# Performance work log

Measured on AMD Instinct MI355X. Metric: run time of the kernel, lower is better.

The kernel has to match this reference:

```python
import jax, jax.numpy as jnp
import numpy as np

ATT_RAW = 312
HID = 900
ATT_DIM = 4096


def setup_inputs() -> dict:
    key = jax.random.key(0)
    ks = jax.random.split(key, 12)
    B, S, N, C = 4, 128, 50, ATT_DIM
    x = jax.random.normal(ks[0], (B, S, C), dtype=jnp.float32)
    x_label = jax.random.randint(ks[1], (B, S), 0, N, dtype=jnp.int64)
    att = jax.random.normal(ks[2], (B, N, ATT_RAW), dtype=jnp.float32)
    att_label = jax.random.randint(ks[3], (B, N), 0, N, dtype=jnp.int64)
    def lin(k, out_f, in_f):
        bound = 1.0 / np.sqrt(in_f)
        kw, kb = jax.random.split(k)
        W = jax.random.uniform(kw, (out_f, in_f), jnp.float32, -bound, bound)
        b = jax.random.uniform(kb, (out_f,), jnp.float32, -bound, bound)
        return W, b
    W1, b1 = lin(ks[4], HID, ATT_RAW)       # attnet layer 1
    W2, b2 = lin(ks[5], ATT_DIM, HID)       # attnet layer 2
    W3, b3 = lin(ks[6], HID, 2 * ATT_DIM)   # o layer 1
    W4, b4 = lin(ks[7], 1, HID)             # o layer 2
    return {"x": x, "x_label": x_label, "att": att, "att_label": att_label,
            "W1": W1, "b1": b1, "W2": W2, "b2": b2,
            "W3": W3, "b3": b3, "W4": W4, "b4": b4}


def reference(x, x_label, att, att_label, W1, b1, W2, b2, W3, b3, W4, b4):
    # x: [B,S,C], att: [B,N,312]; train=True branch -> scalar MSE loss
    B, S, C = x.shape
    N = att.shape[1]
    # attnet: 312 -> 900 -> 4096 with ReLU
    att_f = jax.nn.relu(jax.nn.relu(att @ W1.T + b1) @ W2.T + b2)  # [B,N,4096]
    # o layer 1 on concat([x_f, att_f]) == split matmul + broadcast add
    W3x, W3a = W3[:, :C], W3[:, C:]
    hx = jnp.einsum('bsc,hc->bsh', x, W3x)        # [B,S,900]
    ha = jnp.einsum('bnc,hc->bnh', att_f, W3a)    # [B,N,900]
    pre = jax.nn.relu(hx[:, :, None, :] + ha[:, None, :, :] + b3)  # [B,S,N,900]
    score = jax.nn.sigmoid(jnp.einsum('bsnh,h->bsn', pre, W4[0]) + b4[0])  # [B,S,N]
    label = (x_label[:, :, None] == att_label[:, None, :]).astype(score.dtype)
    loss = jnp.sum((label - score) ** 2) / B / S
    return loss
```

## Files before the change

### kernel.cpp

```cpp
#include <hip/hip_runtime.h>
#include <hip/hip_bf16.h>

typedef __attribute__((ext_vector_type(8))) short bf16x8;
typedef __attribute__((ext_vector_type(4))) float f32x4;
typedef __attribute__((ext_vector_type(8))) unsigned short u16x8;

__device__ __forceinline__ void gload16(const void* g, void* l) {
    __builtin_amdgcn_global_load_lds((const __attribute__((address_space(1))) void*)g,
                                     (__attribute__((address_space(3))) void*)l, 16, 0, 0);
}

__device__ __forceinline__ float bf2f(unsigned short u) {
    union { unsigned i; float f; } v; v.i = ((unsigned)u) << 16; return v.f;
}

struct PadJob {
    const float* src; unsigned short* dst;
    int src_ld, col0, M, K, Kp;
    int chunk_begin;
};
struct PadJobs { PadJob j[6]; int total; };

__global__ __launch_bounds__(256)
void padconv6(PadJobs P)
{
    const int idx = blockIdx.x * 256 + threadIdx.x;
    if (idx >= P.total) return;
    int ji = 0;
    #pragma unroll
    for (int k = 1; k < 6; ++k) if (idx >= P.j[k].chunk_begin) ji = k;
    const PadJob J = P.j[ji];
    const int cid = idx - J.chunk_begin;
    const int kp8 = J.Kp >> 3;
    const int m = cid / kp8;
    const int kc = (cid - m * kp8) << 3;
    u16x8 v;
    if (m < J.M && kc + 8 <= J.K) {
        const float* s = J.src + (size_t)m * J.src_ld + J.col0 + kc;
        const float4 f0 = *(const float4*)s;
        const float4 f1 = *(const float4*)(s + 4);
        const float ff[8] = {f0.x, f0.y, f0.z, f0.w, f1.x, f1.y, f1.z, f1.w};
        #pragma unroll
        for (int j = 0; j < 8; ++j) {
            __hip_bfloat16 h = __float2bfloat16(ff[j]);
            v[j] = *(unsigned short*)&h;
        }
    } else {
        #pragma unroll
        for (int j = 0; j < 8; ++j) {
            float f = 0.f;
            const int k = kc + j;
            if (m < J.M && k < J.K) f = J.src[(size_t)m * J.src_ld + J.col0 + k];
            __hip_bfloat16 h = __float2bfloat16(f);
            v[j] = *(unsigned short*)&h;
        }
    }
    *(u16x8*)(J.dst + (size_t)m * J.Kp + kc) = v;
}

template<bool RELU, bool BIAS>
__global__ __launch_bounds__(256)
void gemm_mfma64(const unsigned short* __restrict__ A,
                 const unsigned short* __restrict__ B,
                 const float* __restrict__ bias,
                 unsigned short* __restrict__ Cout, int ldc,
                 int Mtrue, int Ntrue, int Kp)
{
    __shared__ short As[64 * 64];
    __shared__ short Bs[64 * 64];
    const int bm = blockIdx.y * 64, bn = blockIdx.x * 64;
    const int tid = threadIdx.x;
    const int w = tid >> 6, l = tid & 63;
    const int wm = w >> 1, wn = w & 1;

    const int sr0 = w * 8 + (l >> 3);
    const int scb = (l & 7) * 16;

    f32x4 acc[2][2];
    #pragma unroll
    for (int i = 0; i < 2; ++i)
        #pragma unroll
        for (int j = 0; j < 2; ++j)
            acc[i][j] = (f32x4){0.f, 0.f, 0.f, 0.f};

    for (int k0 = 0; k0 < Kp; k0 += 64) {
        #pragma unroll
        for (int c = 0; c < 2; ++c) {
            const int r = c * 32 + sr0;
            const int cbs = scb ^ ((r & 7) << 4);
            const char* ga = (const char*)(A + (size_t)(bm + r) * Kp + k0) + cbs;
            const char* gb = (const char*)(B + (size_t)(bn + r) * Kp + k0) + cbs;
            char* la = (char*)As + (size_t)(c * 32 + w * 8) * 128;
            char* lb = (char*)Bs + (size_t)(c * 32 + w * 8) * 128;
            gload16(ga, la);
            gload16(gb, lb);
        }
        asm volatile("s_waitcnt vmcnt(0)");
        __syncthreads();

        #pragma unroll
        for (int ks = 0; ks < 64; ks += 32) {
            bf16x8 a[2], b[2];
            const int kb = ks * 2 + (l >> 4) * 16;
            #pragma unroll
            for (int i = 0; i < 2; ++i) {
                const int ra = wm * 32 + i * 16 + (l & 15);
                a[i] = *(const bf16x8*)((const char*)As + ra * 128 + (kb ^ ((ra & 7) << 4)));
                const int rb = wn * 32 + i * 16 + (l & 15);
                b[i] = *(const bf16x8*)((const char*)Bs + rb * 128 + (kb ^ ((rb & 7) << 4)));
            }
            #pragma unroll
            for (int i = 0; i < 2; ++i)
                #pragma unroll
                for (int j = 0; j < 2; ++j)
                    acc[i][j] = __builtin_amdgcn_mfma_f32_16x16x32_bf16(a[i], b[j], acc[i][j], 0, 0, 0);
        }
        __syncthreads();
    }

    #pragma unroll
    for (int i = 0; i < 2; ++i) {
        #pragma unroll
        for (int j = 0; j < 2; ++j) {
            const int col = bn + wn * 32 + j * 16 + (l & 15);
            float bv = 0.f;
            if (BIAS && col < Ntrue) bv = bias[col];
            #pragma unroll
            for (int q = 0; q < 4; ++q) {
                const int row = bm + wm * 32 + i * 16 + (l >> 4) * 4 + q;
                float v = acc[i][j][q] + bv;
                if (RELU) v = fmaxf(v, 0.f);
                if (row >= Mtrue) v = 0.f;
                __hip_bfloat16 h = __float2bfloat16(v);
                Cout[(size_t)row * ldc + col] = *(unsigned short*)&h;
            }
        }
    }
}

struct G34Args {
    const unsigned short *A3, *B3; float* P3;
    const unsigned short *A4, *B4; float* P4;
};

__global__ __launch_bounds__(256)
void gemm128_split(G34Args ga)
{
    __shared__ short As[128 * 64];
    __shared__ short Bs[128 * 64];
    const int tid = threadIdx.x;
    const int w = tid >> 6, l = tid & 63;
    const int wm = w >> 1, wn = w & 1;

    const unsigned short *A, *Bm;
    float* P;
    int by, bx, z, Mtrue;
    const int gid = blockIdx.x;
    if (gid < 256) {
        z = gid >> 5; const int rem = gid & 31; by = rem >> 3; bx = rem & 7;
        A = ga.A3; Bm = ga.B3; P = ga.P3; Mtrue = 512;
    } else {
        const int g2 = gid - 256;
        z = g2 >> 4; const int rem = g2 & 15; by = rem >> 3; bx = rem & 7;
        A = ga.A4; Bm = ga.B4; P = ga.P4; Mtrue = 200;
    }
    const int Kp = 4096;
    const int k_begin = z * 512;

    const int sr0 = w * 8 + (l >> 3);
    const int scb = (l & 7) * 16;
    const int swa = scb ^ ((sr0 & 7) << 4);

    f32x4 acc[4][4];
    #pragma unroll
    for (int i = 0; i < 4; ++i)
        #pragma unroll
        for (int j = 0; j < 4; ++j)
            acc[i][j] = (f32x4){0.f, 0.f, 0.f, 0.f};

    for (int k0 = k_begin; k0 < k_begin + 512; k0 += 64) {
        #pragma unroll
        for (int c = 0; c < 4; ++c) {
            const int r = c * 32 + sr0;
            const char* gA = (const char*)(A  + (size_t)(by * 128 + r) * Kp + k0) + swa;
            const char* gB = (const char*)(Bm + (size_t)(bx * 128 + r) * Kp + k0) + swa;
            char* la = (char*)As + (size_t)(c * 32 + w * 8) * 128;
            char* lb = (char*)Bs + (size_t)(c * 32 + w * 8) * 128;
            gload16(gA, la);
            gload16(gB, lb);
        }
        asm volatile("s_waitcnt vmcnt(0)");
        __syncthreads();

        #pragma unroll
        for (int ks = 0; ks < 64; ks += 32) {
            bf16x8 a[4], b[4];
            const int kb = ks * 2 + (l >> 4) * 16;
            #pragma unroll
            for (int i = 0; i < 4; ++i) {
                const int ra = wm * 64 + i * 16 + (l & 15);
                a[i] = *(const bf16x8*)((const char*)As + ra * 128 + (kb ^ ((ra & 7) << 4)));
                const int rb = wn * 64 + i * 16 + (l & 15);
                b[i] = *(const bf16x8*)((const char*)Bs + rb * 128 + (kb ^ ((rb & 7) << 4)));
            }
            #pragma unroll
            for (int i = 0; i < 4; ++i)
                #pragma unroll
                for (int j = 0; j < 4; ++j)
                    acc[i][j] = __builtin_amdgcn_mfma_f32_16x16x32_bf16(a[i], b[j], acc[i][j], 0, 0, 0);
        }
        __syncthreads();
    }

    float* slab = P + (size_t)z * Mtrue * 900;
    #pragma unroll
    for (int i = 0; i < 4; ++i) {
        #pragma unroll
        for (int j = 0; j < 4; ++j) {
            const int col = bx * 128 + wn * 64 + j * 16 + (l & 15);
            if (col >= 900) continue;
            #pragma unroll
            for (int q = 0; q < 4; ++q) {
                const int row = by * 128 + wm * 64 + i * 16 + (l >> 4) * 4 + q;
                if (row < Mtrue)
                    slab[(size_t)row * 900 + col] = acc[i][j][q];
            }
        }
    }
}

__global__ __launch_bounds__(256)
void reduce_both(const float* __restrict__ hxp, const float* __restrict__ hap,
                 const float* __restrict__ b3,
                 unsigned short* __restrict__ hx_bf, unsigned short* __restrict__ ha_bf)
{
    int idx = blockIdx.x * 256 + threadIdx.x;
    const int HX = 512 * 113;
    const float* p; unsigned short* o; const float* bias; int M, m;
    if (idx < HX) { p = hxp; o = hx_bf; bias = b3; M = 512; }
    else {
        idx -= HX;
        if (idx >= 200 * 113) return;
        p = hap; o = ha_bf; bias = nullptr; M = 200;
    }
    m = idx / 113;
    const int c = idx - m * 113;
    const int k = c * 8;
    u16x8 v;
    #pragma unroll
    for (int q = 0; q < 8; q += 4) {
        if (k + q < 900) {
            float4 a = *(const float4*)(p + (size_t)m * 900 + k + q);
            #pragma unroll 1
            for (int s = 1; s < 8; ++s) {
                const float4 t = *(const float4*)(p + ((size_t)s * M + m) * 900 + k + q);
                a.x += t.x; a.y += t.y; a.z += t.z; a.w += t.w;
            }
            if (bias) {
                const float4 bb = *(const float4*)(bias + k + q);
                a.x += bb.x; a.y += bb.y; a.z += bb.z; a.w += bb.w;
            }
            const float ff[4] = {a.x, a.y, a.z, a.w};
            #pragma unroll
            for (int j = 0; j < 4; ++j) {
                __hip_bfloat16 h = __float2bfloat16(ff[j]);
                v[q + j] = *(unsigned short*)&h;
            }
        } else {
            #pragma unroll
            for (int j = 0; j < 4; ++j) v[q + j] = 0;
        }
    }
    *(u16x8*)(o + (size_t)m * 904 + k) = v;
}

__global__ __launch_bounds__(512)
void score_loss(const unsigned short* __restrict__ hxb,
                const unsigned short* __restrict__ hab,
                const float* __restrict__ W4,
                const float* __restrict__ b4,
                const int* __restrict__ xl,
                const int* __restrict__ al,
                float* __restrict__ part)
{
    __shared__ __align__(16) unsigned short hxs[8 * 904];
    __shared__ __align__(16) unsigned short has[16 * 904];
    __shared__ __align__(16) float w4s[904];
    __shared__ float zpart[4][8][16];
    __shared__ float red[2];

    const int tid = threadIdx.x;
    const int nt = blockIdx.x, st = blockIdx.y, b = blockIdx.z;
    const int row0 = b * 128 + st * 8;

    for (int t = tid; t < 24 * 113; t += 512) {
        u16x8 v;
        unsigned short* dst;
        if (t < 8 * 113) {
            const int r = t / 113, c = t - r * 113;
            v = *(const u16x8*)(hxb + (size_t)(row0 + r) * 904 + c * 8);
            dst = hxs + r * 904 + c * 8;
        } else {
            const int t2 = t - 8 * 113;
            const int r = t2 / 113, c = t2 - r * 113;
            const int n = nt * 16 + r;
            if (n < 50) v = *(const u16x8*)(hab + (size_t)(b * 50 + n) * 904 + c * 8);
            else        v = (u16x8){0,0,0,0,0,0,0,0};
            dst = has + r * 904 + c * 8;
        }
        *(u16x8*)dst = v;
    }
    for (int t = tid; t < 226; t += 512) {
        float4 v = {0.f, 0.f, 0.f, 0.f};
        if (t < 225) v = *(const float4*)(W4 + t * 4);
        *(float4*)(w4s + t * 4) = v;
    }
    __syncthreads();

    const int hs = tid >> 7;
    const int si = (tid >> 4) & 7;
    const int ni = tid & 15;

    float acc = 0.f;
    const unsigned short* hrow = hxs + si * 904;
    const unsigned short* arow = has + ni * 904;
    for (int c = hs; c < 113; c += 4) {
        const u16x8 hv = *(const u16x8*)(hrow + c * 8);
        const u16x8 av = *(const u16x8*)(arow + c * 8);
        const float4 w0 = *(const float4*)(w4s + c * 8);
        const float4 w1 = *(const float4*)(w4s + c * 8 + 4);
        const float ww[8] = {w0.x, w0.y, w0.z, w0.w, w1.x, w1.y, w1.z, w1.w};
        #pragma unroll
        for (int j = 0; j < 8; ++j) {
            const float u = bf2f((unsigned short)hv[j]) + bf2f((unsigned short)av[j]);
            acc = fmaf(fmaxf(u, 0.f), ww[j], acc);
        }
    }
    zpart[hs][si][ni] = acc;
    __syncthreads();

    float dd = 0.f;
    if (tid < 128) {
        const int esi = tid >> 4, eni = tid & 15;
        const int n = nt * 16 + eni;
        const float z = zpart[0][esi][eni] + zpart[1][esi][eni]
                      + zpart[2][esi][eni] + zpart[3][esi][eni] + b4[0];
        const float sc = 1.f / (1.f + __expf(-z));
        if (n < 50) {
            const float lab = (xl[row0 + esi] == al[b * 50 + n]) ? 1.f : 0.f;
            const float d = lab - sc;
            dd = d * d;
        }
        #pragma unroll
        for (int off = 32; off > 0; off >>= 1)
            dd += __shfl_down(dd, off);
        if ((tid & 63) == 0) red[tid >> 6] = dd;
    }
    __syncthreads();
    if (tid == 0)
        part[nt + 4 * (st + 16 * b)] = red[0] + red[1];
}

__global__ __launch_bounds__(256)
void final_loss(const float* __restrict__ part, float* __restrict__ out)
{
    __shared__ float r[4];
    const int tid = threadIdx.x;
    float v = part[tid];
    #pragma unroll
    for (int off = 32; off > 0; off >>= 1)
        v += __shfl_down(v, off);
    if ((tid & 63) == 0) r[tid >> 6] = v;
    __syncthreads();
    if (tid == 0) out[0] = (r[0] + r[1] + r[2] + r[3]) * (1.f / 512.f);
}

extern "C" void kernel_launch(void* const* d_in, const int* in_sizes, int n_in,
                              void* d_out, int out_size, void* d_ws, size_t ws_size,
                              hipStream_t stream)
{
    const float* x   = (const float*)d_in[0];
    const int*   xl  = (const int*)  d_in[1];
    const float* att = (const float*)d_in[2];
    const int*   al  = (const int*)  d_in[3];
    const float* W1  = (const float*)d_in[4];
    const float* b1  = (const float*)d_in[5];
    const float* W2  = (const float*)d_in[6];
    const float* b2  = (const float*)d_in[7];
    const float* W3  = (const float*)d_in[8];
    const float* b3  = (const float*)d_in[9];
    const float* W4  = (const float*)d_in[10];
    const float* b4  = (const float*)d_in[11];
    float* out = (float*)d_out;

    const int B = 4, S = 128, N = 50, C = 4096, H = 900, AR = 312;
    const int MS = B * S;
    const int MN = B * N;
    const int MNp = 256;
    const int ARp = 320, Hp = 960;
    const int W3p = 1024;
    const int SPLITS = 8;

    char* base = (char*)d_ws;
    size_t off = 0;
    auto alloc = [&](size_t bytes) { void* r = base + off; off = (off + bytes + 255) & ~(size_t)255; return r; };
    unsigned short* x_bf   = (unsigned short*)alloc((size_t)MS * C * 2);
    unsigned short* att_bf = (unsigned short*)alloc((size_t)MNp * ARp * 2);
    unsigned short* W1_bf  = (unsigned short*)alloc((size_t)Hp * ARp * 2);
    unsigned short* W2_bf  = (unsigned short*)alloc((size_t)C * Hp * 2);
    unsigned short* W3x_bf = (unsigned short*)alloc((size_t)W3p * C * 2);
    unsigned short* W3a_bf = (unsigned short*)alloc((size_t)W3p * C * 2);
    unsigned short* h1_bf  = (unsigned short*)alloc((size_t)MNp * Hp * 2);
    unsigned short* attf_bf= (unsigned short*)alloc((size_t)MNp * C * 2);
    float* hxp = (float*)alloc((size_t)SPLITS * MS * H * 4);
    float* hap = (float*)alloc((size_t)SPLITS * MN * H * 4);
    unsigned short* hx_bf = (unsigned short*)alloc((size_t)MS * 904 * 2);
    unsigned short* ha_bf = (unsigned short*)alloc((size_t)MN * 904 * 2);
    float* part = (float*)alloc(256 * 4);

    const dim3 blk(256);
    auto cdiv = [](int a, int b) { return (a + b - 1) / b; };

    PadJobs P;
    int cb = 0;
    auto setjob = [&](int i, const float* src, unsigned short* dst, int ld, int col0,
                      int M, int K, int Kp, int Mp) {
        P.j[i] = PadJob{src, dst, ld, col0, M, K, Kp, cb};
        cb += Mp * (Kp >> 3);
    };
    setjob(0, x,   x_bf,   C,     0, MS, C,  C,   MS);
    setjob(1, att, att_bf, AR,    0, MN, AR, ARp, MNp);
    setjob(2, W1,  W1_bf,  AR,    0, H,  AR, ARp, Hp);
    setjob(3, W2,  W2_bf,  H,     0, C,  H,  Hp,  C);
    setjob(4, W3,  W3x_bf, 2 * C, 0, H,  C,  C,   W3p);
    setjob(5, W3,  W3a_bf, 2 * C, C, H,  C,  C,   W3p);
    P.total = cb;
    padconv6<<<cdiv(cb, 256), blk, 0, stream>>>(P);

    gemm_mfma64<true, true><<<dim3(Hp / 64, MNp / 64), blk, 0, stream>>>(
        att_bf, W1_bf, b1, h1_bf, Hp, MN, H, ARp);

    gemm_mfma64<true, true><<<dim3(C / 64, MNp / 64), blk, 0, stream>>>(
        h1_bf, W2_bf, b2, attf_bf, C, MN, C, Hp);

    G34Args ga{x_bf, W3x_bf, hxp, attf_bf, W3a_bf, hap};
    gemm128_split<<<dim3(384), blk, 0, stream>>>(ga);

    reduce_both<<<cdiv((MS + MN) * 113, 256), blk, 0, stream>>>(hxp, hap, b3, hx_bf, ha_bf);

    score_loss<<<dim3(4, 16, 4), dim3(512), 0, stream>>>(hx_bf, ha_bf, W4, b4, xl, al, part);
    final_loss<<<dim3(1), blk, 0, stream>>>(part, out);
}
```

Measured before the change: 71.24 us.

## Fuse fp32-to-bf16 conversion and padding into GEMM tile staging

Removes the separate padconv6 pre-pass that converted x, att, W1, W2 and W3 into padded bf16 workspace copies. Each GEMM now reads the fp32 (or bf16) source directly, converts and zero-pads in registers, and writes into swizzled LDS. This avoids a full extra write and read of about 30 MB of converted data and one kernel launch. In exchange it drops the asynchronous global_load_lds path for ordinary register-staged loads with bounds checks, and the fp32 sources double the bytes read per tile.

```diff
diff --git a/kernel.cpp b/kernel.cpp
--- a/kernel.cpp
+++ b/kernel.cpp
@@ -5,63 +5,58 @@
 typedef __attribute__((ext_vector_type(4))) float f32x4;
 typedef __attribute__((ext_vector_type(8))) unsigned short u16x8;
 
-__device__ __forceinline__ void gload16(const void* g, void* l) {
-    __builtin_amdgcn_global_load_lds((const __attribute__((address_space(1))) void*)g,
-                                     (__attribute__((address_space(3))) void*)l, 16, 0, 0);
-}
-
 __device__ __forceinline__ float bf2f(unsigned short u) {
     union { unsigned i; float f; } v; v.i = ((unsigned)u) << 16; return v.f;
 }
-
-struct PadJob {
-    const float* src; unsigned short* dst;
-    int src_ld, col0, M, K, Kp;
-    int chunk_begin;
-};
-struct PadJobs { PadJob j[6]; int total; };
-
-__global__ __launch_bounds__(256)
-void padconv6(PadJobs P)
-{
-    const int idx = blockIdx.x * 256 + threadIdx.x;
-    if (idx >= P.total) return;
-    int ji = 0;
-    #pragma unroll
-    for (int k = 1; k < 6; ++k) if (idx >= P.j[k].chunk_begin) ji = k;
-    const PadJob J = P.j[ji];
-    const int cid = idx - J.chunk_begin;
-    const int kp8 = J.Kp >> 3;
-    const int m = cid / kp8;
-    const int kc = (cid - m * kp8) << 3;
-    u16x8 v;
-    if (m < J.M && kc + 8 <= J.K) {
-        const float* s = J.src + (size_t)m * J.src_ld + J.col0 + kc;
-        const float4 f0 = *(const float4*)s;
-        const float4 f1 = *(const float4*)(s + 4);
-        const float ff[8] = {f0.x, f0.y, f0.z, f0.w, f1.x, f1.y, f1.z, f1.w};
-        #pragma unroll
-        for (int j = 0; j < 8; ++j) {
-            __hip_bfloat16 h = __float2bfloat16(ff[j]);
-            v[j] = *(unsigned short*)&h;
-        }
-    } else {
-        #pragma unroll
-        for (int j = 0; j < 8; ++j) {
-            float f = 0.f;
-            const int k = kc + j;
-            if (m < J.M && k < J.K) f = J.src[(size_t)m * J.src_ld + J.col0 + k];
-            __hip_bfloat16 h = __float2bfloat16(f);
-            v[j] = *(unsigned short*)&h;
-        }
-    }
-    *(u16x8*)(J.dst + (size_t)m * J.Kp + kc) = v;
+__device__ __forceinline__ unsigned short f2bf(float f) {
+    __hip_bfloat16 h = __float2bfloat16(f);
+    return *(unsigned short*)&h;
+}
+
+template<int ROWS>
+__device__ __forceinline__ void stage_tile(
+    const void* __restrict__ src, int ld, int isbf, int row0, int rmax,
+    int k0, int kmax, short* __restrict__ lds, int tid)
+{
+    #pragma unroll
+    for (int i = 0; i < ROWS / 32; ++i) {
+        const int ch = i * 256 + tid;
+        const int r = ch >> 3;
+        const int kc8 = (ch & 7) * 8;
+        const int gr = row0 + r;
+        const int gk = k0 + kc8;
+        u16x8 v;
+        if (gr < rmax && gk + 8 <= kmax) {
+            if (isbf) {
+                v = *(const u16x8*)((const unsigned short*)src + (size_t)gr * ld + gk);
+            } else {
+                const float* s = (const float*)src + (size_t)gr * ld + gk;
+                const float4 f0 = *(const float4*)s;
+                const float4 f1 = *(const float4*)(s + 4);
+                const float ff[8] = {f0.x, f0.y, f0.z, f0.w, f1.x, f1.y, f1.z, f1.w};
+                #pragma unroll
+                for (int j = 0; j < 8; ++j) v[j] = f2bf(ff[j]);
+            }
+        } else if (gr < rmax && gk < kmax) {
+            #pragma unroll
+            for (int j = 0; j < 8; ++j) {
+                float f = 0.f;
+                if (gk + j < kmax)
+                    f = isbf ? bf2f(((const unsigned short*)src)[(size_t)gr * ld + gk + j])
+                             : ((const float*)src)[(size_t)gr * ld + gk + j];
+                v[j] = f2bf(f);
+            }
+        } else {
+            v = (u16x8){0, 0, 0, 0, 0, 0, 0, 0};
+        }
+        *(u16x8*)((char*)lds + r * 128 + ((kc8 * 2) ^ ((r & 7) << 4))) = v;
+    }
 }
 
 template<bool RELU, bool BIAS>
 __global__ __launch_bounds__(256)
-void gemm_mfma64(const unsigned short* __restrict__ A,
-                 const unsigned short* __restrict__ B,
+void gemm_mfma64(const void* __restrict__ A, int lda, int a_bf, int a_rmax, int a_kmax,
+                 const void* __restrict__ B, int ldb, int b_bf, int b_rmax, int b_kmax,
                  const float* __restrict__ bias,
                  unsigned short* __restrict__ Cout, int ldc,
                  int Mtrue, int Ntrue, int Kp)
@@ -73,9 +68,6 @@
     const int w = tid >> 6, l = tid & 63;
     const int wm = w >> 1, wn = w & 1;
 
-    const int sr0 = w * 8 + (l >> 3);
-    const int scb = (l & 7) * 16;
-
     f32x4 acc[2][2];
     #pragma unroll
     for (int i = 0; i < 2; ++i)
@@ -84,18 +76,8 @@
             acc[i][j] = (f32x4){0.f, 0.f, 0.f, 0.f};
 
     for (int k0 = 0; k0 < Kp; k0 += 64) {
-        #pragma unroll
-        for (int c = 0; c < 2; ++c) {
-            const int r = c * 32 + sr0;
-            const int cbs = scb ^ ((r & 7) << 4);
-            const char* ga = (const char*)(A + (size_t)(bm + r) * Kp + k0) + cbs;
-            const char* gb = (const char*)(B + (size_t)(bn + r) * Kp + k0) + cbs;
-            char* la = (char*)As + (size_t)(c * 32 + w * 8) * 128;
-            char* lb = (char*)Bs + (size_t)(c * 32 + w * 8) * 128;
-            gload16(ga, la);
-            gload16(gb, lb);
-        }
-        asm volatile("s_waitcnt vmcnt(0)");
+        stage_tile<64>(A, lda, a_bf, bm, a_rmax, k0, a_kmax, As, tid);
+        stage_tile<64>(B, ldb, b_bf, bn, b_rmax, k0, b_kmax, Bs, tid);
         __syncthreads();
 
         #pragma unroll
@@ -131,16 +113,15 @@
                 float v = acc[i][j][q] + bv;
                 if (RELU) v = fmaxf(v, 0.f);
                 if (row >= Mtrue) v = 0.f;
-                __hip_bfloat16 h = __float2bfloat16(v);
-                Cout[(size_t)row * ldc + col] = *(unsigned short*)&h;
+                Cout[(size_t)row * ldc + col] = f2bf(v);
             }
         }
     }
 }
 
 struct G34Args {
-    const unsigned short *A3, *B3; float* P3;
-    const unsigned short *A4, *B4; float* P4;
+    const void *A3; const float *B3; float* P3;
+    const void *A4; const float *B4; float* P4;
 };
 
 __global__ __launch_bounds__(256)
@@ -152,24 +133,19 @@
     const int w = tid >> 6, l = tid & 63;
     const int wm = w >> 1, wn = w & 1;
 
-    const unsigned short *A, *Bm;
+    const void *A; const float *Bm;
     float* P;
-    int by, bx, z, Mtrue;
+    int by, bx, z, Mtrue, a_bf, a_rmax, lda;
     const int gid = blockIdx.x;
     if (gid < 256) {
         z = gid >> 5; const int rem = gid & 31; by = rem >> 3; bx = rem & 7;
-        A = ga.A3; Bm = ga.B3; P = ga.P3; Mtrue = 512;
+        A = ga.A3; Bm = ga.B3; P = ga.P3; Mtrue = 512; a_bf = 0; a_rmax = 512; lda = 4096;
     } else {
         const int g2 = gid - 256;
         z = g2 >> 4; const int rem = g2 & 15; by = rem >> 3; bx = rem & 7;
-        A = ga.A4; Bm = ga.B4; P = ga.P4; Mtrue = 200;
-    }
-    const int Kp = 4096;
+        A = ga.A4; Bm = ga.B4; P = ga.P4; Mtrue = 200; a_bf = 1; a_rmax = 256; lda = 4096;
+    }
     const int k_begin = z * 512;
-
-    const int sr0 = w * 8 + (l >> 3);
-    const int scb = (l & 7) * 16;
-    const int swa = scb ^ ((sr0 & 7) << 4);
 
     f32x4 acc[4][4];
     #pragma unroll
@@ -179,17 +155,8 @@
             acc[i][j] = (f32x4){0.f, 0.f, 0.f, 0.f};
 
     for (int k0 = k_begin; k0 < k_begin + 512; k0 += 64) {
-        #pragma unroll
-        for (int c = 0; c < 4; ++c) {
-            const int r = c * 32 + sr0;
-            const char* gA = (const char*)(A  + (size_t)(by * 128 + r) * Kp + k0) + swa;
-            const char* gB = (const char*)(Bm + (size_t)(bx * 128 + r) * Kp + k0) + swa;
-            char* la = (char*)As + (size_t)(c * 32 + w * 8) * 128;
-            char* lb = (char*)Bs + (size_t)(c * 32 + w * 8) * 128;
-            gload16(gA, la);
-            gload16(gB, lb);
-        }
-        asm volatile("s_waitcnt vmcnt(0)");
+        stage_tile<128>(A, lda, a_bf, by * 128, a_rmax, k0, 4096, As, tid);
+        stage_tile<128>(Bm, 8192, 0, bx * 128, 900, k0, 1 << 30, Bs, tid);
         __syncthreads();
 
         #pragma unroll
@@ -260,12 +227,8 @@
                 const float4 bb = *(const float4*)(bias + k + q);
                 a.x += bb.x; a.y += bb.y; a.z += bb.z; a.w += bb.w;
             }
-            const float ff[4] = {a.x, a.y, a.z, a.w};
-            #pragma unroll
-            for (int j = 0; j < 4; ++j) {
-                __hip_bfloat16 h = __float2bfloat16(ff[j]);
-                v[q + j] = *(unsigned short*)&h;
-            }
+            v[q + 0] = f2bf(a.x); v[q + 1] = f2bf(a.y);
+            v[q + 2] = f2bf(a.z); v[q + 3] = f2bf(a.w);
         } else {
             #pragma unroll
             for (int j = 0; j < 4; ++j) v[q + j] = 0;
@@ -398,18 +361,11 @@
     const int MN = B * N;
     const int MNp = 256;
     const int ARp = 320, Hp = 960;
-    const int W3p = 1024;
     const int SPLITS = 8;
 
     char* base = (char*)d_ws;
     size_t off = 0;
     auto alloc = [&](size_t bytes) { void* r = base + off; off = (off + bytes + 255) & ~(size_t)255; return r; };
-    unsigned short* x_bf   = (unsigned short*)alloc((size_t)MS * C * 2);
-    unsigned short* att_bf = (unsigned short*)alloc((size_t)MNp * ARp * 2);
-    unsigned short* W1_bf  = (unsigned short*)alloc((size_t)Hp * ARp * 2);
-    unsigned short* W2_bf  = (unsigned short*)alloc((size_t)C * Hp * 2);
-    unsigned short* W3x_bf = (unsigned short*)alloc((size_t)W3p * C * 2);
-    unsigned short* W3a_bf = (unsigned short*)alloc((size_t)W3p * C * 2);
     unsigned short* h1_bf  = (unsigned short*)alloc((size_t)MNp * Hp * 2);
     unsigned short* attf_bf= (unsigned short*)alloc((size_t)MNp * C * 2);
     float* hxp = (float*)alloc((size_t)SPLITS * MS * H * 4);
@@ -421,29 +377,17 @@
     const dim3 blk(256);
     auto cdiv = [](int a, int b) { return (a + b - 1) / b; };
 
-    PadJobs P;
-    int cb = 0;
-    auto setjob = [&](int i, const float* src, unsigned short* dst, int ld, int col0,
-                      int M, int K, int Kp, int Mp) {
-        P.j[i] = PadJob{src, dst, ld, col0, M, K, Kp, cb};
-        cb += Mp * (Kp >> 3);
-    };
-    setjob(0, x,   x_bf,   C,     0, MS, C,  C,   MS);
-    setjob(1, att, att_bf, AR,    0, MN, AR, ARp, MNp);
-    setjob(2, W1,  W1_bf,  AR,    0, H,  AR, ARp, Hp);
-    setjob(3, W2,  W2_bf,  H,     0, C,  H,  Hp,  C);
-    setjob(4, W3,  W3x_bf, 2 * C, 0, H,  C,  C,   W3p);
-    setjob(5, W3,  W3a_bf, 2 * C, C, H,  C,  C,   W3p);
-    P.total = cb;
-    padconv6<<<cdiv(cb, 256), blk, 0, stream>>>(P);
-
     gemm_mfma64<true, true><<<dim3(Hp / 64, MNp / 64), blk, 0, stream>>>(
-        att_bf, W1_bf, b1, h1_bf, Hp, MN, H, ARp);
+        att, AR, 0, MN, AR,
+        W1,  AR, 0, H,  AR,
+        b1, h1_bf, Hp, MN, H, ARp);
 
     gemm_mfma64<true, true><<<dim3(C / 64, MNp / 64), blk, 0, stream>>>(
-        h1_bf, W2_bf, b2, attf_bf, C, MN, C, Hp);
-
-    G34Args ga{x_bf, W3x_bf, hxp, attf_bf, W3a_bf, hap};
+        h1_bf, Hp, 1, MNp, Hp,
+        W2,    H,  0, C,   H,
+        b2, attf_bf, C, MN, C, Hp);
+
+    G34Args ga{x, W3, hxp, attf_bf, W3 + C, hap};
     gemm128_split<<<dim3(384), blk, 0, stream>>>(ga);
 
     reduce_both<<<cdiv((MS + MN) * 113, 256), blk, 0, stream>>>(hxp, hap, b3, hx_bf, ha_bf);
```

Measured after the change: 94.22 us. 32.2% more time.

## Double-buffer LDS in GEMM kernels and raise split-K for the x-side GEMM

Applied to the files above, without the earlier changes.

Both MFMA GEMM kernels now use two LDS buffers and issue the global-to-LDS loads for the next K tile before computing the current one, so memory latency overlaps with MFMA work. The x-side GEMM in the split kernel goes from 8 to 16 K-splits (640 blocks instead of 384), which adds parallelism across CUs. The cost is twice the fp32 partial-sum traffic and reduction work for hx, plus higher LDS use per block (64KB in the split kernel), which may lower occupancy.

```diff
diff --git a/kernel.cpp b/kernel.cpp
--- a/kernel.cpp
+++ b/kernel.cpp
@@ -9,9 +9,12 @@
     __builtin_amdgcn_global_load_lds((const __attribute__((address_space(1))) void*)g,
                                      (__attribute__((address_space(3))) void*)l, 16, 0, 0);
 }
-
 __device__ __forceinline__ float bf2f(unsigned short u) {
     union { unsigned i; float f; } v; v.i = ((unsigned)u) << 16; return v.f;
+}
+__device__ __forceinline__ unsigned short f2bf(float f) {
+    __hip_bfloat16 h = __float2bfloat16(f);
+    return *(unsigned short*)&h;
 }
 
 struct PadJob {
@@ -41,21 +44,34 @@
         const float4 f1 = *(const float4*)(s + 4);
         const float ff[8] = {f0.x, f0.y, f0.z, f0.w, f1.x, f1.y, f1.z, f1.w};
         #pragma unroll
-        for (int j = 0; j < 8; ++j) {
-            __hip_bfloat16 h = __float2bfloat16(ff[j]);
-            v[j] = *(unsigned short*)&h;
-        }
+        for (int j = 0; j < 8; ++j) v[j] = f2bf(ff[j]);
     } else {
         #pragma unroll
         for (int j = 0; j < 8; ++j) {
             float f = 0.f;
             const int k = kc + j;
             if (m < J.M && k < J.K) f = J.src[(size_t)m * J.src_ld + J.col0 + k];
-            __hip_bfloat16 h = __float2bfloat16(f);
-            v[j] = *(unsigned short*)&h;
+            v[j] = f2bf(f);
         }
     }
     *(u16x8*)(J.dst + (size_t)m * J.Kp + kc) = v;
+}
+
+template<int ROWS>
+__device__ __forceinline__ void stage_gl(const unsigned short* __restrict__ src,
+                                         int ld, int row0, int k0,
+                                         short* __restrict__ lds, int w, int l)
+{
+    const int sr0 = w * 8 + (l >> 3);
+    const int scb = (l & 7) * 16;
+    #pragma unroll
+    for (int c = 0; c < ROWS / 32; ++c) {
+        const int r = c * 32 + sr0;
+        const int cbs = scb ^ ((r & 7) << 4);
+        const char* g = (const char*)(src + (size_t)(row0 + r) * ld + k0) + cbs;
+        char* dst = (char*)lds + (size_t)(c * 32 + w * 8) * 128;
+        gload16(g, dst);
+    }
 }
 
 template<bool RELU, bool BIAS>
@@ -66,15 +82,13 @@
                  unsigned short* __restrict__ Cout, int ldc,
                  int Mtrue, int Ntrue, int Kp)
 {
-    __shared__ short As[64 * 64];
-    __shared__ short Bs[64 * 64];
+    __shared__ short As[2][64 * 64];
+    __shared__ short Bs[2][64 * 64];
     const int bm = blockIdx.y * 64, bn = blockIdx.x * 64;
     const int tid = threadIdx.x;
     const int w = tid >> 6, l = tid & 63;
     const int wm = w >> 1, wn = w & 1;
-
-    const int sr0 = w * 8 + (l >> 3);
-    const int scb = (l & 7) * 16;
+    const int nk = Kp >> 6;
 
     f32x4 acc[2][2];
     #pragma unroll
@@ -83,21 +97,17 @@
         for (int j = 0; j < 2; ++j)
             acc[i][j] = (f32x4){0.f, 0.f, 0.f, 0.f};
 
-    for (int k0 = 0; k0 < Kp; k0 += 64) {
-        #pragma unroll
-        for (int c = 0; c < 2; ++c) {
-            const int r = c * 32 + sr0;
-            const int cbs = scb ^ ((r & 7) << 4);
-            const char* ga = (const char*)(A + (size_t)(bm + r) * Kp + k0) + cbs;
-            const char* gb = (const char*)(B + (size_t)(bn + r) * Kp + k0) + cbs;
-            char* la = (char*)As + (size_t)(c * 32 + w * 8) * 128;
-            char* lb = (char*)Bs + (size_t)(c * 32 + w * 8) * 128;
-            gload16(ga, la);
-            gload16(gb, lb);
-        }
-        asm volatile("s_waitcnt vmcnt(0)");
-        __syncthreads();
-
+    stage_gl<64>(A, Kp, bm, 0, As[0], w, l);
+    stage_gl<64>(B, Kp, bn, 0, Bs[0], w, l);
+    asm volatile("s_waitcnt vmcnt(0)");
+    __syncthreads();
+
+    int cur = 0;
+    for (int t = 0; t < nk; ++t) {
+        if (t + 1 < nk) {
+            stage_gl<64>(A, Kp, bm, (t + 1) * 64, As[cur ^ 1], w, l);
+            stage_gl<64>(B, Kp, bn, (t + 1) * 64, Bs[cur ^ 1], w, l);
+        }
         #pragma unroll
         for (int ks = 0; ks < 64; ks += 32) {
             bf16x8 a[2], b[2];
@@ -105,9 +115,9 @@
             #pragma unroll
             for (int i = 0; i < 2; ++i) {
                 const int ra = wm * 32 + i * 16 + (l & 15);
-                a[i] = *(const bf16x8*)((const char*)As + ra * 128 + (kb ^ ((ra & 7) << 4)));
+                a[i] = *(const bf16x8*)((const char*)As[cur] + ra * 128 + (kb ^ ((ra & 7) << 4)));
                 const int rb = wn * 32 + i * 16 + (l & 15);
-                b[i] = *(const bf16x8*)((const char*)Bs + rb * 128 + (kb ^ ((rb & 7) << 4)));
+                b[i] = *(const bf16x8*)((const char*)Bs[cur] + rb * 128 + (kb ^ ((rb & 7) << 4)));
             }
             #pragma unroll
             for (int i = 0; i < 2; ++i)
@@ -115,7 +125,9 @@
                 for (int j = 0; j < 2; ++j)
                     acc[i][j] = __builtin_amdgcn_mfma_f32_16x16x32_bf16(a[i], b[j], acc[i][j], 0, 0, 0);
         }
+        asm volatile("s_waitcnt vmcnt(0)");
         __syncthreads();
+        cur ^= 1;
     }
 
     #pragma unroll
@@ -131,8 +143,7 @@
                 float v = acc[i][j][q] + bv;
                 if (RELU) v = fmaxf(v, 0.f);
                 if (row >= Mtrue) v = 0.f;
-                __hip_bfloat16 h = __float2bfloat16(v);
-                Cout[(size_t)row * ldc + col] = *(unsigned short*)&h;
+                Cout[(size_t)row * ldc + col] = f2bf(v);
             }
         }
     }
@@ -146,30 +157,26 @@
 __global__ __launch_bounds__(256)
 void gemm128_split(G34Args ga)
 {
-    __shared__ short As[128 * 64];
-    __shared__ short Bs[128 * 64];
+    __shared__ short As[2][128 * 64];
+    __shared__ short Bs[2][128 * 64];
     const int tid = threadIdx.x;
     const int w = tid >> 6, l = tid & 63;
     const int wm = w >> 1, wn = w & 1;
 
     const unsigned short *A, *Bm;
     float* P;
-    int by, bx, z, Mtrue;
+    int by, bx, z, Mtrue, nk, k_begin;
     const int gid = blockIdx.x;
-    if (gid < 256) {
-        z = gid >> 5; const int rem = gid & 31; by = rem >> 3; bx = rem & 7;
+    if (gid < 512) {
+        z = gid >> 5; by = (gid >> 3) & 3; bx = gid & 7;
         A = ga.A3; Bm = ga.B3; P = ga.P3; Mtrue = 512;
+        nk = 4; k_begin = z * 256;
     } else {
-        const int g2 = gid - 256;
-        z = g2 >> 4; const int rem = g2 & 15; by = rem >> 3; bx = rem & 7;
+        const int g2 = gid - 512;
+        z = g2 >> 4; by = (g2 >> 3) & 1; bx = g2 & 7;
         A = ga.A4; Bm = ga.B4; P = ga.P4; Mtrue = 200;
-    }
-    const int Kp = 4096;
-    const int k_begin = z * 512;
-
-    const int sr0 = w * 8 + (l >> 3);
-    const int scb = (l & 7) * 16;
-    const int swa = scb ^ ((sr0 & 7) << 4);
+        nk = 8; k_begin = z * 512;
+    }
 
     f32x4 acc[4][4];
     #pragma unroll
@@ -178,20 +185,17 @@
         for (int j = 0; j < 4; ++j)
             acc[i][j] = (f32x4){0.f, 0.f, 0.f, 0.f};
 
-    for (int k0 = k_begin; k0 < k_begin + 512; k0 += 64) {
-        #pragma unroll
-        for (int c = 0; c < 4; ++c) {
-            const int r = c * 32 + sr0;
-            const char* gA = (const char*)(A  + (size_t)(by * 128 + r) * Kp + k0) + swa;
-            const char* gB = (const char*)(Bm + (size_t)(bx * 128 + r) * Kp + k0) + swa;
-            char* la = (char*)As + (size_t)(c * 32 + w * 8) * 128;
-            char* lb = (char*)Bs + (size_t)(c * 32 + w * 8) * 128;
-            gload16(gA, la);
-            gload16(gB, lb);
-        }
-        asm volatile("s_waitcnt vmcnt(0)");
-        __syncthreads();
-
+    stage_gl<128>(A, 4096, by * 128, k_begin, As[0], w, l);
+    stage_gl<128>(Bm, 4096, bx * 128, k_begin, Bs[0], w, l);
+    asm volatile("s_waitcnt vmcnt(0)");
+    __syncthreads();
+
+    int cur = 0;
+    for (int t = 0; t < nk; ++t) {
+        if (t + 1 < nk) {
+            stage_gl<128>(A, 4096, by * 128, k_begin + (t + 1) * 64, As[cur ^ 1], w, l);
+            stage_gl<128>(Bm, 4096, bx * 128, k_begin + (t + 1) * 64, Bs[cur ^ 1], w, l);
+        }
         #pragma unroll
         for (int ks = 0; ks < 64; ks += 32) {
             bf16x8 a[4], b[4];
@@ -199,9 +203,9 @@
             #pragma unroll
             for (int i = 0; i < 4; ++i) {
                 const int ra = wm * 64 + i * 16 + (l & 15);
-                a[i] = *(const bf16x8*)((const char*)As + ra * 128 + (kb ^ ((ra & 7) << 4)));
+                a[i] = *(const bf16x8*)((const char*)As[cur] + ra * 128 + (kb ^ ((ra & 7) << 4)));
                 const int rb = wn * 64 + i * 16 + (l & 15);
-                b[i] = *(const bf16x8*)((const char*)Bs + rb * 128 + (kb ^ ((rb & 7) << 4)));
+                b[i] = *(const bf16x8*)((const char*)Bs[cur] + rb * 128 + (kb ^ ((rb & 7) << 4)));
             }
             #pragma unroll
             for (int i = 0; i < 4; ++i)
@@ -209,7 +213,9 @@
                 for (int j = 0; j < 4; ++j)
                     acc[i][j] = __builtin_amdgcn_mfma_f32_16x16x32_bf16(a[i], b[j], acc[i][j], 0, 0, 0);
         }
+        asm volatile("s_waitcnt vmcnt(0)");
         __syncthreads();
+        cur ^= 1;
     }
 
     float* slab = P + (size_t)z * Mtrue * 900;
@@ -236,14 +242,14 @@
 {
     int idx = blockIdx.x * 256 + threadIdx.x;
     const int HX = 512 * 113;
-    const float* p; unsigned short* o; const float* bias; int M, m;
-    if (idx < HX) { p = hxp; o = hx_bf; bias = b3; M = 512; }
+    const float* p; unsigned short* o; const float* bias; int M, ns;
+    if (idx < HX) { p = hxp; o = hx_bf; bias = b3; M = 512; ns = 16; }
     else {
         idx -= HX;
         if (idx >= 200 * 113) return;
-        p = hap; o = ha_bf; bias = nullptr; M = 200;
-    }
-    m = idx / 113;
+        p = hap; o = ha_bf; bias = nullptr; M = 200; ns = 8;
+    }
+    const int m = idx / 113;
     const int c = idx - m * 113;
     const int k = c * 8;
     u16x8 v;
@@ -252,7 +258,7 @@
         if (k + q < 900) {
             float4 a = *(const float4*)(p + (size_t)m * 900 + k + q);
             #pragma unroll 1
-            for (int s = 1; s < 8; ++s) {
+            for (int s = 1; s < ns; ++s) {
                 const float4 t = *(const float4*)(p + ((size_t)s * M + m) * 900 + k + q);
                 a.x += t.x; a.y += t.y; a.z += t.z; a.w += t.w;
             }
@@ -260,12 +266,8 @@
                 const float4 bb = *(const float4*)(bias + k + q);
                 a.x += bb.x; a.y += bb.y; a.z += bb.z; a.w += bb.w;
             }
-            const float ff[4] = {a.x, a.y, a.z, a.w};
-            #pragma unroll
-            for (int j = 0; j < 4; ++j) {
-                __hip_bfloat16 h = __float2bfloat16(ff[j]);
-                v[q + j] = *(unsigned short*)&h;
-            }
+            v[q + 0] = f2bf(a.x); v[q + 1] = f2bf(a.y);
+            v[q + 2] = f2bf(a.z); v[q + 3] = f2bf(a.w);
         } else {
             #pragma unroll
             for (int j = 0; j < 4; ++j) v[q + j] = 0;
@@ -399,7 +401,7 @@
     const int MNp = 256;
     const int ARp = 320, Hp = 960;
     const int W3p = 1024;
-    const int SPLITS = 8;
+    const int SPL3 = 16, SPL4 = 8;
 
     char* base = (char*)d_ws;
     size_t off = 0;
@@ -412,8 +414,8 @@
     unsigned short* W3a_bf = (unsigned short*)alloc((size_t)W3p * C * 2);
     unsigned short* h1_bf  = (unsigned short*)alloc((size_t)MNp * Hp * 2);
     unsigned short* attf_bf= (unsigned short*)alloc((size_t)MNp * C * 2);
-    float* hxp = (float*)alloc((size_t)SPLITS * MS * H * 4);
-    float* hap = (float*)alloc((size_t)SPLITS * MN * H * 4);
+    float* hxp = (float*)alloc((size_t)SPL3 * MS * H * 4);
+    float* hap = (float*)alloc((size_t)SPL4 * MN * H * 4);
     unsigned short* hx_bf = (unsigned short*)alloc((size_t)MS * 904 * 2);
     unsigned short* ha_bf = (unsigned short*)alloc((size_t)MN * 904 * 2);
     float* part = (float*)alloc(256 * 4);
@@ -444,7 +446,7 @@
         h1_bf, W2_bf, b2, attf_bf, C, MN, C, Hp);
 
     G34Args ga{x_bf, W3x_bf, hxp, attf_bf, W3a_bf, hap};
-    gemm128_split<<<dim3(384), blk, 0, stream>>>(ga);
+    gemm128_split<<<dim3(640), blk, 0, stream>>>(ga);
 
     reduce_both<<<cdiv((MS + MN) * 113, 256), blk, 0, stream>>>(hxp, hap, b3, hx_bf, ha_bf);
 
```

Measured after the change: 84.23 us. +18.2%, slower.

## Fuse first attnet GEMM into pad kernel and split-K reduce into score kernel

Applied to the files above, without the earlier changes.

The first GEMM (att x W1) now runs in the same launch as the bf16 conversion kernel. Its blocks stage fp32 inputs directly into LDS with on-the-fly bf16 conversion, so att and W1 no longer need padded copies. The separate split-K reduction kernel is removed, and score_loss now sums the 8 fp32 partials plus bias while loading its tiles. This removes two kernel launches and the hx/ha bf16 intermediate round trips. In exchange, each score_loss block redundantly re-reads partials: hx rows are reloaded for every n-tile and ha rows for every s-tile, which increases global reads.

```diff
diff --git a/kernel.cpp b/kernel.cpp
--- a/kernel.cpp
+++ b/kernel.cpp
@@ -9,9 +9,63 @@
     __builtin_amdgcn_global_load_lds((const __attribute__((address_space(1))) void*)g,
                                      (__attribute__((address_space(3))) void*)l, 16, 0, 0);
 }
-
 __device__ __forceinline__ float bf2f(unsigned short u) {
     union { unsigned i; float f; } v; v.i = ((unsigned)u) << 16; return v.f;
+}
+__device__ __forceinline__ unsigned short f2bf(float f) {
+    __hip_bfloat16 h = __float2bfloat16(f);
+    return *(unsigned short*)&h;
+}
+
+template<int ROWS>
+__device__ __forceinline__ void stage_f32(
+    const float* __restrict__ src, int ld, int row0, int rmax,
+    int k0, int kmax, short* __restrict__ lds, int tid)
+{
+    #pragma unroll
+    for (int i = 0; i < ROWS / 32; ++i) {
+        const int ch = i * 256 + tid;
+        const int r = ch >> 3;
+        const int kc8 = (ch & 7) * 8;
+        const int gr = row0 + r;
+        const int gk = k0 + kc8;
+        u16x8 v;
+        if (gr < rmax && gk + 8 <= kmax) {
+            const float* s = src + (size_t)gr * ld + gk;
+            const float4 f0 = *(const float4*)s;
+            const float4 f1 = *(const float4*)(s + 4);
+            const float ff[8] = {f0.x, f0.y, f0.z, f0.w, f1.x, f1.y, f1.z, f1.w};
+            #pragma unroll
+            for (int j = 0; j < 8; ++j) v[j] = f2bf(ff[j]);
+        } else if (gr < rmax && gk < kmax) {
+            #pragma unroll
+            for (int j = 0; j < 8; ++j) {
+                float f = 0.f;
+                if (gk + j < kmax) f = src[(size_t)gr * ld + gk + j];
+                v[j] = f2bf(f);
+            }
+        } else {
+            v = (u16x8){0, 0, 0, 0, 0, 0, 0, 0};
+        }
+        *(u16x8*)((char*)lds + r * 128 + ((kc8 * 2) ^ ((r & 7) << 4))) = v;
+    }
+}
+
+template<int ROWS>
+__device__ __forceinline__ void stage_gl(const unsigned short* __restrict__ src,
+                                         int ld, int row0, int k0,
+                                         short* __restrict__ lds, int w, int l)
+{
+    const int sr0 = w * 8 + (l >> 3);
+    const int scb = (l & 7) * 16;
+    #pragma unroll
+    for (int c = 0; c < ROWS / 32; ++c) {
+        const int r = c * 32 + sr0;
+        const int cbs = scb ^ ((r & 7) << 4);
+        const char* g = (const char*)(src + (size_t)(row0 + r) * ld + k0) + cbs;
+        char* dst = (char*)lds + (size_t)(c * 32 + w * 8) * 128;
+        gload16(g, dst);
+    }
 }
 
 struct PadJob {
@@ -19,16 +73,79 @@
     int src_ld, col0, M, K, Kp;
     int chunk_begin;
 };
-struct PadJobs { PadJob j[6]; int total; };
+struct PG1Args {
+    PadJob j[4]; int total;
+    const float *att, *W1, *b1;
+    unsigned short* h1;
+};
 
 __global__ __launch_bounds__(256)
-void padconv6(PadJobs P)
-{
-    const int idx = blockIdx.x * 256 + threadIdx.x;
+void padg1(PG1Args P)
+{
+    __shared__ short As[64 * 64];
+    __shared__ short Bs[64 * 64];
+    const int gid = blockIdx.x;
+    const int tid = threadIdx.x;
+
+    if (gid < 60) {
+        const int bm = (gid & 3) * 64, bn = (gid >> 2) * 64;
+        const int w = tid >> 6, l = tid & 63;
+        const int wm = w >> 1, wn = w & 1;
+
+        f32x4 acc[2][2];
+        #pragma unroll
+        for (int i = 0; i < 2; ++i)
+            #pragma unroll
+            for (int j = 0; j < 2; ++j)
+                acc[i][j] = (f32x4){0.f, 0.f, 0.f, 0.f};
+
+        for (int k0 = 0; k0 < 320; k0 += 64) {
+            stage_f32<64>(P.att, 312, bm, 200, k0, 312, As, tid);
+            stage_f32<64>(P.W1,  312, bn, 900, k0, 312, Bs, tid);
+            __syncthreads();
+            #pragma unroll
+            for (int ks = 0; ks < 64; ks += 32) {
+                bf16x8 a[2], b[2];
+                const int kb = ks * 2 + (l >> 4) * 16;
+                #pragma unroll
+                for (int i = 0; i < 2; ++i) {
+                    const int ra = wm * 32 + i * 16 + (l & 15);
+                    a[i] = *(const bf16x8*)((const char*)As + ra * 128 + (kb ^ ((ra & 7) << 4)));
+                    const int rb = wn * 32 + i * 16 + (l & 15);
+                    b[i] = *(const bf16x8*)((const char*)Bs + rb * 128 + (kb ^ ((rb & 7) << 4)));
+                }
+                #pragma unroll
+                for (int i = 0; i < 2; ++i)
+                    #pragma unroll
+                    for (int j = 0; j < 2; ++j)
+                        acc[i][j] = __builtin_amdgcn_mfma_f32_16x16x32_bf16(a[i], b[j], acc[i][j], 0, 0, 0);
+            }
+            __syncthreads();
+        }
+
+        #pragma unroll
+        for (int i = 0; i < 2; ++i) {
+            #pragma unroll
+            for (int j = 0; j < 2; ++j) {
+                const int col = bn + wn * 32 + j * 16 + (l & 15);
+                const float bv = (col < 900) ? P.b1[col] : 0.f;
+                #pragma unroll
+                for (int q = 0; q < 4; ++q) {
+                    const int row = bm + wm * 32 + i * 16 + (l >> 4) * 4 + q;
+                    float v = fmaxf(acc[i][j][q] + bv, 0.f);
+                    if (row >= 200) v = 0.f;
+                    P.h1[(size_t)row * 960 + col] = f2bf(v);
+                }
+            }
+        }
+        return;
+    }
+
+    const int idx = (gid - 60) * 256 + tid;
     if (idx >= P.total) return;
     int ji = 0;
     #pragma unroll
-    for (int k = 1; k < 6; ++k) if (idx >= P.j[k].chunk_begin) ji = k;
+    for (int k = 1; k < 4; ++k) if (idx >= P.j[k].chunk_begin) ji = k;
     const PadJob J = P.j[ji];
     const int cid = idx - J.chunk_begin;
     const int kp8 = J.Kp >> 3;
@@ -41,18 +158,14 @@
         const float4 f1 = *(const float4*)(s + 4);
         const float ff[8] = {f0.x, f0.y, f0.z, f0.w, f1.x, f1.y, f1.z, f1.w};
         #pragma unroll
-        for (int j = 0; j < 8; ++j) {
-            __hip_bfloat16 h = __float2bfloat16(ff[j]);
-            v[j] = *(unsigned short*)&h;
-        }
+        for (int j = 0; j < 8; ++j) v[j] = f2bf(ff[j]);
     } else {
         #pragma unroll
         for (int j = 0; j < 8; ++j) {
             float f = 0.f;
             const int k = kc + j;
             if (m < J.M && k < J.K) f = J.src[(size_t)m * J.src_ld + J.col0 + k];
-            __hip_bfloat16 h = __float2bfloat16(f);
-            v[j] = *(unsigned short*)&h;
+            v[j] = f2bf(f);
         }
     }
     *(u16x8*)(J.dst + (size_t)m * J.Kp + kc) = v;
@@ -73,9 +186,6 @@
     const int w = tid >> 6, l = tid & 63;
     const int wm = w >> 1, wn = w & 1;
 
-    const int sr0 = w * 8 + (l >> 3);
-    const int scb = (l & 7) * 16;
-
     f32x4 acc[2][2];
     #pragma unroll
     for (int i = 0; i < 2; ++i)
@@ -84,17 +194,8 @@
             acc[i][j] = (f32x4){0.f, 0.f, 0.f, 0.f};
 
     for (int k0 = 0; k0 < Kp; k0 += 64) {
-        #pragma unroll
-        for (int c = 0; c < 2; ++c) {
-            const int r = c * 32 + sr0;
-            const int cbs = scb ^ ((r & 7) << 4);
-            const char* ga = (const char*)(A + (size_t)(bm + r) * Kp + k0) + cbs;
-            const char* gb = (const char*)(B + (size_t)(bn + r) * Kp + k0) + cbs;
-            char* la = (char*)As + (size_t)(c * 32 + w * 8) * 128;
-            char* lb = (char*)Bs + (size_t)(c * 32 + w * 8) * 128;
-            gload16(ga, la);
-            gload16(gb, lb);
-        }
+        stage_gl<64>(A, Kp, bm, k0, As, w, l);
+        stage_gl<64>(B, Kp, bn, k0, Bs, w, l);
         asm volatile("s_waitcnt vmcnt(0)");
         __syncthreads();
 
@@ -131,8 +232,7 @@
                 float v = acc[i][j][q] + bv;
                 if (RELU) v = fmaxf(v, 0.f);
                 if (row >= Mtrue) v = 0.f;
-                __hip_bfloat16 h = __float2bfloat16(v);
-                Cout[(size_t)row * ldc + col] = *(unsigned short*)&h;
+                Cout[(size_t)row * ldc + col] = f2bf(v);
             }
         }
     }
@@ -164,12 +264,7 @@
         z = g2 >> 4; const int rem = g2 & 15; by = rem >> 3; bx = rem & 7;
         A = ga.A4; Bm = ga.B4; P = ga.P4; Mtrue = 200;
     }
-    const int Kp = 4096;
     const int k_begin = z * 512;
-
-    const int sr0 = w * 8 + (l >> 3);
-    const int scb = (l & 7) * 16;
-    const int swa = scb ^ ((sr0 & 7) << 4);
 
     f32x4 acc[4][4];
     #pragma unroll
@@ -179,16 +274,8 @@
             acc[i][j] = (f32x4){0.f, 0.f, 0.f, 0.f};
 
     for (int k0 = k_begin; k0 < k_begin + 512; k0 += 64) {
-        #pragma unroll
-        for (int c = 0; c < 4; ++c) {
-            const int r = c * 32 + sr0;
-            const char* gA = (const char*)(A  + (size_t)(by * 128 + r) * Kp + k0) + swa;
-            const char* gB = (const char*)(Bm + (size_t)(bx * 128 + r) * Kp + k0) + swa;
-            char* la = (char*)As + (size_t)(c * 32 + w * 8) * 128;
-            char* lb = (char*)Bs + (size_t)(c * 32 + w * 8) * 128;
-            gload16(gA, la);
-            gload16(gB, lb);
-        }
+        stage_gl<128>(A, 4096, by * 128, k0, As, w, l);
+        stage_gl<128>(Bm, 4096, bx * 128, k0, Bs, w, l);
         asm volatile("s_waitcnt vmcnt(0)");
         __syncthreads();
 
@@ -229,54 +316,10 @@
     }
 }
 
-__global__ __launch_bounds__(256)
-void reduce_both(const float* __restrict__ hxp, const float* __restrict__ hap,
-                 const float* __restrict__ b3,
-                 unsigned short* __restrict__ hx_bf, unsigned short* __restrict__ ha_bf)
-{
-    int idx = blockIdx.x * 256 + threadIdx.x;
-    const int HX = 512 * 113;
-    const float* p; unsigned short* o; const float* bias; int M, m;
-    if (idx < HX) { p = hxp; o = hx_bf; bias = b3; M = 512; }
-    else {
-        idx -= HX;
-        if (idx >= 200 * 113) return;
-        p = hap; o = ha_bf; bias = nullptr; M = 200;
-    }
-    m = idx / 113;
-    const int c = idx - m * 113;
-    const int k = c * 8;
-    u16x8 v;
-    #pragma unroll
-    for (int q = 0; q < 8; q += 4) {
-        if (k + q < 900) {
-            float4 a = *(const float4*)(p + (size_t)m * 900 + k + q);
-            #pragma unroll 1
-            for (int s = 1; s < 8; ++s) {
-                const float4 t = *(const float4*)(p + ((size_t)s * M + m) * 900 + k + q);
-                a.x += t.x; a.y += t.y; a.z += t.z; a.w += t.w;
-            }
-            if (bias) {
-                const float4 bb = *(const float4*)(bias + k + q);
-                a.x += bb.x; a.y += bb.y; a.z += bb.z; a.w += bb.w;
-            }
-            const float ff[4] = {a.x, a.y, a.z, a.w};
-            #pragma unroll
-            for (int j = 0; j < 4; ++j) {
-                __hip_bfloat16 h = __float2bfloat16(ff[j]);
-                v[q + j] = *(unsigned short*)&h;
-            }
-        } else {
-            #pragma unroll
-            for (int j = 0; j < 4; ++j) v[q + j] = 0;
-        }
-    }
-    *(u16x8*)(o + (size_t)m * 904 + k) = v;
-}
-
 __global__ __launch_bounds__(512)
-void score_loss(const unsigned short* __restrict__ hxb,
-                const unsigned short* __restrict__ hab,
+void score_loss(const float* __restrict__ hxp,
+                const float* __restrict__ hap,
+                const float* __restrict__ b3,
                 const float* __restrict__ W4,
                 const float* __restrict__ b4,
                 const int* __restrict__ xl,
@@ -294,20 +337,56 @@
     const int row0 = b * 128 + st * 8;
 
     for (int t = tid; t < 24 * 113; t += 512) {
-        u16x8 v;
+        float f[8] = {0.f, 0.f, 0.f, 0.f, 0.f, 0.f, 0.f, 0.f};
         unsigned short* dst;
+        int nv;
         if (t < 8 * 113) {
             const int r = t / 113, c = t - r * 113;
-            v = *(const u16x8*)(hxb + (size_t)(row0 + r) * 904 + c * 8);
-            dst = hxs + r * 904 + c * 8;
+            const int k = c * 8;
+            nv = (k + 8 <= 900) ? 8 : 4;
+            const int row = row0 + r;
+            #pragma unroll 1
+            for (int s = 0; s < 8; ++s) {
+                const float* p = hxp + ((size_t)s * 512 + row) * 900 + k;
+                const float4 a0 = *(const float4*)p;
+                f[0] += a0.x; f[1] += a0.y; f[2] += a0.z; f[3] += a0.w;
+                if (nv == 8) {
+                    const float4 a1 = *(const float4*)(p + 4);
+                    f[4] += a1.x; f[5] += a1.y; f[6] += a1.z; f[7] += a1.w;
+                }
+            }
+            const float4 bb0 = *(const float4*)(b3 + k);
+            f[0] += bb0.x; f[1] += bb0.y; f[2] += bb0.z; f[3] += bb0.w;
+            if (nv == 8) {
+                const float4 bb1 = *(const float4*)(b3 + k + 4);
+                f[4] += bb1.x; f[5] += bb1.y; f[6] += bb1.z; f[7] += bb1.w;
+            }
+            dst = hxs + r * 904 + k;
         } else {
             const int t2 = t - 8 * 113;
             const int r = t2 / 113, c = t2 - r * 113;
+            const int k = c * 8;
+            nv = (k + 8 <= 900) ? 8 : 4;
             const int n = nt * 16 + r;
-            if (n < 50) v = *(const u16x8*)(hab + (size_t)(b * 50 + n) * 904 + c * 8);
-            else        v = (u16x8){0,0,0,0,0,0,0,0};
-            dst = has + r * 904 + c * 8;
-        }
+            if (n < 50) {
+                const int row = b * 50 + n;
+                #pragma unroll 1
+                for (int s = 0; s < 8; ++s) {
+                    const float* p = hap + ((size_t)s * 200 + row) * 900 + k;
+                    const float4 a0 = *(const float4*)p;
+                    f[0] += a0.x; f[1] += a0.y; f[2] += a0.z; f[3] += a0.w;
+                    if (nv == 8) {
+                        const float4 a1 = *(const float4*)(p + 4);
+                        f[4] += a1.x; f[5] += a1.y; f[6] += a1.z; f[7] += a1.w;
+                    }
+                }
+            }
+            dst = has + r * 904 + k;
+        }
+        u16x8 v;
+        #pragma unroll
+        for (int j = 0; j < 8; ++j) v[j] = f2bf(f[j]);
+        if (nv == 4) { v[4] = 0; v[5] = 0; v[6] = 0; v[7] = 0; }
         *(u16x8*)dst = v;
     }
     for (int t = tid; t < 226; t += 512) {
@@ -397,7 +476,7 @@
     const int MS = B * S;
     const int MN = B * N;
     const int MNp = 256;
-    const int ARp = 320, Hp = 960;
+    const int Hp = 960;
     const int W3p = 1024;
     const int SPLITS = 8;
 
@@ -405,8 +484,6 @@
     size_t off = 0;
     auto alloc = [&](size_t bytes) { void* r = base + off; off = (off + bytes + 255) & ~(size_t)255; return r; };
     unsigned short* x_bf   = (unsigned short*)alloc((size_t)MS * C * 2);
-    unsigned short* att_bf = (unsigned short*)alloc((size_t)MNp * ARp * 2);
-    unsigned short* W1_bf  = (unsigned short*)alloc((size_t)Hp * ARp * 2);
     unsigned short* W2_bf  = (unsigned short*)alloc((size_t)C * Hp * 2);
     unsigned short* W3x_bf = (unsigned short*)alloc((size_t)W3p * C * 2);
     unsigned short* W3a_bf = (unsigned short*)alloc((size_t)W3p * C * 2);
@@ -414,14 +491,12 @@
     unsigned short* attf_bf= (unsigned short*)alloc((size_t)MNp * C * 2);
     float* hxp = (float*)alloc((size_t)SPLITS * MS * H * 4);
     float* hap = (float*)alloc((size_t)SPLITS * MN * H * 4);
-    unsigned short* hx_bf = (unsigned short*)alloc((size_t)MS * 904 * 2);
-    unsigned short* ha_bf = (unsigned short*)alloc((size_t)MN * 904 * 2);
     float* part = (float*)alloc(256 * 4);
 
     const dim3 blk(256);
     auto cdiv = [](int a, int b) { return (a + b - 1) / b; };
 
-    PadJobs P;
+    PG1Args P;
     int cb = 0;
     auto setjob = [&](int i, const float* src, unsigned short* dst, int ld, int col0,
                       int M, int K, int Kp, int Mp) {
@@ -429,16 +504,12 @@
         cb += Mp * (Kp >> 3);
     };
     setjob(0, x,   x_bf,   C,     0, MS, C,  C,   MS);
-    setjob(1, att, att_bf, AR,    0, MN, AR, ARp, MNp);
-    setjob(2, W1,  W1_bf,  AR,    0, H,  AR, ARp, Hp);
-    setjob(3, W2,  W2_bf,  H,     0, C,  H,  Hp,  C);
-    setjob(4, W3,  W3x_bf, 2 * C, 0, H,  C,  C,   W3p);
-    setjob(5, W3,  W3a_bf, 2 * C, C, H,  C,  C,   W3p);
+    setjob(1, W2,  W2_bf,  H,     0, C,  H,  Hp,  C);
+    setjob(2, W3,  W3x_bf, 2 * C, 0, H,  C,  C,   W3p);
+    setjob(3, W3,  W3a_bf, 2 * C, C, H,  C,  C,   W3p);
     P.total = cb;
-    padconv6<<<cdiv(cb, 256), blk, 0, stream>>>(P);
-
-    gemm_mfma64<true, true><<<dim3(Hp / 64, MNp / 64), blk, 0, stream>>>(
-        att_bf, W1_bf, b1, h1_bf, Hp, MN, H, ARp);
+    P.att = att; P.W1 = W1; P.b1 = b1; P.h1 = h1_bf;
+    padg1<<<dim3(60 + cdiv(cb, 256)), blk, 0, stream>>>(P);
 
     gemm_mfma64<true, true><<<dim3(C / 64, MNp / 64), blk, 0, stream>>>(
         h1_bf, W2_bf, b2, attf_bf, C, MN, C, Hp);
@@ -446,8 +517,6 @@
     G34Args ga{x_bf, W3x_bf, hxp, attf_bf, W3a_bf, hap};
     gemm128_split<<<dim3(384), blk, 0, stream>>>(ga);
 
-    reduce_both<<<cdiv((MS + MN) * 113, 256), blk, 0, stream>>>(hxp, hap, b3, hx_bf, ha_bf);
-
-    score_loss<<<dim3(4, 16, 4), dim3(512), 0, stream>>>(hx_bf, ha_bf, W4, b4, xl, al, part);
+    score_loss<<<dim3(4, 16, 4), dim3(512), 0, stream>>>(hxp, hap, b3, W4, b4, xl, al, part);
     final_loss<<<dim3(1), blk, 0, stream>>>(part, out);
 }
```

Result: slower. 82.63 us (+16.0%).
